# Optimization experiments

Measured on AMD Instinct MI355X. Metric: run time of the kernel, lower is better.

## Reference

```python
import jax, jax.numpy as jnp
import numpy as np

N = 50000          # num nodes
E = 600000         # num edges
D_IN = 128         # node_dim
D_HID = 128        # hidden_dim
D_OUT = 32         # num_classes
R = 32             # num_relations
B = 8              # num_bases


def setup_inputs() -> dict:
    key = jax.random.key(0)
    ks = jax.random.split(key, 12)
    inp = {
        "x": jax.random.normal(ks[0], (N, D_IN), dtype=jnp.float32),
        "V1": jax.random.normal(ks[1], (B, D_IN, D_HID), dtype=jnp.float32) * 0.05,
        "a1": jax.random.normal(ks[2], (R, B), dtype=jnp.float32),
        "root1": jax.random.normal(ks[3], (D_IN, D_HID), dtype=jnp.float32) * 0.05,
        "bias1": jnp.zeros((D_HID,), dtype=jnp.float32),
        "V2": jax.random.normal(ks[4], (B, D_HID, D_OUT), dtype=jnp.float32) * 0.05,
        "a2": jax.random.normal(ks[5], (R, B), dtype=jnp.float32),
        "root2": jax.random.normal(ks[6], (D_HID, D_OUT), dtype=jnp.float32) * 0.05,
        "bias2": jnp.zeros((D_OUT,), dtype=jnp.float32),
        "edge_index": jax.random.randint(ks[7], (2, E), 0, N, dtype=jnp.int64),
        "edge_type": jax.random.randint(ks[8], (E,), 0, R, dtype=jnp.int64),
    }
    return inp


def rgcn_layer(x, V, a, root, bias, src, dst, etype):
    # Aggregate neighbor features per (relation, dst-node) with mean norm,
    # then apply basis-decomposed relation weights W_r = sum_b a[r,b] V_b.
    D = x.shape[-1]
    seg = etype * N + dst                                   # [E] combined segment id
    msgs = x[src]                                           # [E, D] gather
    agg = jax.ops.segment_sum(msgs, seg, num_segments=R * N)        # [R*N, D]
    cnt = jax.ops.segment_sum(jnp.ones((msgs.shape[0], 1), x.dtype), seg,
                              num_segments=R * N)                   # [R*N, 1]
    agg = (agg / jnp.maximum(cnt, 1.0)).reshape(R, N, D)            # [R, N, D]
    W = jnp.einsum('rb,bdo->rdo', a, V)                     # [R, D, Dout]
    out = jnp.einsum('rnd,rdo->no', agg, W) + x @ root + bias
    return out


def reference(x, V1, a1, root1, bias1, V2, a2, root2, bias2, edge_index, edge_type):
    src, dst = edge_index[0], edge_index[1]
    h = rgcn_layer(x, V1, a1, root1, bias1, src, dst, edge_type)
    h = jax.nn.relu(h)
    h = rgcn_layer(h, V2, a2, root2, bias2, src, dst, edge_type)
    return jax.nn.softmax(h, axis=1)
```

## Files before the change

### kernel.cpp

```cpp
#include <hip/hip_runtime.h>
#include <hip/hip_bf16.h>
#include <hip/hip_fp16.h>


typedef __attribute__((ext_vector_type(8))) short bf16x8;
typedef __attribute__((ext_vector_type(4))) float f32x4;
typedef unsigned short u16;
typedef __attribute__((ext_vector_type(4))) unsigned short u16x4;

constexpr int TD   = 128;
constexpr int TB   = 8;
constexpr int TK   = TB * TD;
constexpr int TNB  = 16;
constexpr int BLK  = 512;
constexpr int ZK   = TK + 8;
constexpr int XK   = TD + 8;
constexpr int EC   = 512;

__device__ inline unsigned int splitbf(float v) {
  unsigned int u = __float_as_uint(v);
  unsigned int r = u + 0x7FFF + ((u >> 16) & 1);
  unsigned int hb = r >> 16;
  float hv = __uint_as_float(hb << 16);
  float lo = v - hv;
  unsigned int u2 = __float_as_uint(lo);
  unsigned int r2 = u2 + 0x7FFF + ((u2 >> 16) & 1);
  return (hb & 0xFFFFu) | (r2 & 0xFFFF0000u);
}

__device__ inline u16 f2h(float v) { return __half_as_ushort(__float2half(v)); }
__device__ inline float h2f(u16 b) { return __half2float(__ushort_as_half(b)); }

__global__ void k_prep(const float* __restrict__ V1, const float* __restrict__ root1,
                       const float* __restrict__ V2, const float* __restrict__ root2,
                       u16* __restrict__ v1th, u16* __restrict__ v1tl,
                       u16* __restrict__ r1th, u16* __restrict__ r1tl,
                       u16* __restrict__ v2th, u16* __restrict__ v2tl,
                       u16* __restrict__ r2th, u16* __restrict__ r2tl) {
  int idx = blockIdx.x * 256 + threadIdx.x;
  if (idx < 128 * 1024) {
    unsigned int p = splitbf(V1[(size_t)(idx & 1023) * 128 + (idx >> 10)]);
    v1th[idx] = (u16)p; v1tl[idx] = (u16)(p >> 16);
  }
  if (idx < 128 * 128) {
    unsigned int p = splitbf(root1[(size_t)(idx & 127) * 128 + (idx >> 7)]);
    r1th[idx] = (u16)p; r1tl[idx] = (u16)(p >> 16);
  }
  if (idx < 32 * 1024) {
    unsigned int p = splitbf(V2[(size_t)(idx & 1023) * 32 + (idx >> 10)]);
    v2th[idx] = (u16)p; v2tl[idx] = (u16)(p >> 16);
  }
  if (idx < 32 * 128) {
    unsigned int p = splitbf(root2[(size_t)(idx & 127) * 32 + (idx >> 7)]);
    r2th[idx] = (u16)p; r2tl[idx] = (u16)(p >> 16);
  }
}

__global__ void k_xcast(const float* __restrict__ x, u16* __restrict__ xb, int n4) {
  int i = blockIdx.x * 256 + threadIdx.x;
  if (i >= n4) return;
  float4 v = reinterpret_cast<const float4*>(x)[i];
  u16x4 o;
  o[0] = f2h(v.x); o[1] = f2h(v.y); o[2] = f2h(v.z); o[3] = f2h(v.w);
  reinterpret_cast<u16x4*>(xb)[i] = o;
}

__global__ void k_hist(const int* __restrict__ ei, const int* __restrict__ et,
                       int* __restrict__ deg, int* __restrict__ cnt2,
                       int E, int N) {
  int e = blockIdx.x * 256 + threadIdx.x;
  if (e >= E) return;
  int d = ei[E + e];
  int r = et[e];
  atomicAdd(&deg[d], 1);
  atomicAdd(&cnt2[r * N + d], 1);
}

__global__ void k_scan(const int* __restrict__ deg, int* __restrict__ off,
                       int* __restrict__ cursor, int n, int total) {
  __shared__ int wsum[16];
  __shared__ int carry_s;
  const int t = threadIdx.x, lane = t & 63, w = t >> 6;
  if (t == 0) carry_s = 0;
  __syncthreads();
  for (int base = 0; base < n; base += 1024) {
    int i = base + t;
    int v = (i < n) ? deg[i] : 0;
    int s = v;
#pragma unroll
    for (int d = 1; d < 64; d <<= 1) {
      int u = __shfl_up(s, d);
      if (lane >= d) s += u;
    }
    if (lane == 63) wsum[w] = s;
    __syncthreads();
    if (w == 0) {
      int ws = (lane < 16) ? wsum[lane] : 0;
#pragma unroll
      for (int d = 1; d < 16; d <<= 1) {
        int u = __shfl_up(ws, d);
        if (lane >= d) ws += u;
      }
      if (lane < 16) wsum[lane] = ws;
    }
    __syncthreads();
    int wbase = (w == 0) ? 0 : wsum[w - 1];
    int carry = carry_s;
    if (i < n) { int ex = carry + wbase + s - v; off[i] = ex; cursor[i] = ex; }
    __syncthreads();
    if (t == 1023) carry_s = carry + wbase + s;
    __syncthreads();
  }
  if (t == 0) off[n] = total;
}

__global__ void k_scatter(const int* __restrict__ ei, const int* __restrict__ et,
                          int* __restrict__ cursor, const int* __restrict__ cnt2,
                          int* __restrict__ packed, float* __restrict__ invc,
                          int E, int N) {
  int e = blockIdx.x * 256 + threadIdx.x;
  if (e >= E) return;
  int s = ei[e], d = ei[E + e], r = et[e];
  int p = atomicAdd(&cursor[d], 1);
  packed[p] = s | (r << 17);
  invc[p] = 1.0f / (float)cnt2[r * N + d];
}

#define MFMA16(A, B, C) __builtin_amdgcn_mfma_f32_16x16x32_bf16((A), (B), (C), 0, 0, 0)

template <int DOUT, bool RELU, bool SOFTMAX, bool INF32, bool OUTH16>
__global__ __launch_bounds__(BLK, 4) void k_layer(
    const float* __restrict__ inf,
    const u16* __restrict__ inb,
    const u16* __restrict__ wth, const u16* __restrict__ wtl,
    const float* __restrict__ a,
    const u16* __restrict__ rth, const u16* __restrict__ rtl,
    const float* __restrict__ bias, const int* __restrict__ off,
    const int* __restrict__ packed, const float* __restrict__ invc,
    void* __restrict__ outv, int Ntot) {
  extern __shared__ char smem[];
  u16* zh = (u16*)smem;
  u16* zl = zh + TNB * ZK;
  u16* xh = zl + TNB * ZK;
  u16* xl2 = xh + TNB * XK;
  float* ash = (float*)(xl2 + TNB * XK);
  int*   lrp = (int*)(ash + 256);
  float* lri = (float*)(lrp + EC);
  const int t = threadIdx.x;
  const int n0 = blockIdx.x * TNB;

  if (t < 256) ash[t] = a[t];
  {
    int row = t >> 5;
    int c4 = (t & 31) * 4;
    int n = n0 + row;
    float4 v = make_float4(0.f, 0.f, 0.f, 0.f);
    if constexpr (INF32) {
      if (n < Ntot) v = *reinterpret_cast<const float4*>(inf + (size_t)n * TD + c4);
    } else {
      if (n < Ntot) {
        u16x4 hv = *reinterpret_cast<const u16x4*>(inb + (size_t)n * TD + c4);
        v = make_float4(h2f(hv[0]), h2f(hv[1]), h2f(hv[2]), h2f(hv[3]));
      }
    }
    unsigned int p0 = splitbf(v.x), p1 = splitbf(v.y), p2 = splitbf(v.z), p3 = splitbf(v.w);
    xh[row * XK + c4]     = (u16)p0; xl2[row * XK + c4]     = (u16)(p0 >> 16);
    xh[row * XK + c4 + 1] = (u16)p1; xl2[row * XK + c4 + 1] = (u16)(p1 >> 16);
    xh[row * XK + c4 + 2] = (u16)p2; xl2[row * XK + c4 + 2] = (u16)(p2 >> 16);
    xh[row * XK + c4 + 3] = (u16)p3; xl2[row * XK + c4 + 3] = (u16)(p3 >> 16);
  }
  const int e_start = off[n0 < Ntot ? n0 : Ntot];
  {
    int nend = n0 + TNB; if (nend > Ntot) nend = Ntot;
    int ec = off[nend] - e_start;
    if (ec > EC) ec = EC;
    for (int i = t; i < ec; i += BLK) {
      lrp[i] = packed[e_start + i];
      lri[i] = invc[e_start + i];
    }
  }
  __syncthreads();

  {
    const int wv = t >> 6, lane = t & 63;
    const int hf = lane >> 5, q = lane & 31;

    for (int nn = wv * 2; nn < wv * 2 + 2; ++nn) {
      int n = n0 + nn;
      float acc[8][4];
#pragma unroll
      for (int b = 0; b < 8; ++b)
#pragma unroll
        for (int j = 0; j < 4; ++j) acc[b][j] = 0.f;

      if (n < Ntot) {
        int e0 = off[n], e1 = off[n + 1];
        int np = (e1 - e0 + 1) >> 1;

        struct Pk { float4 xv, c0, c1; };
        auto ldst = [&](int pe) {
          Pk P;
          int e = e0 + 2 * pe + hf;
          float iv = 0.f; int r = 0;
          u16x4 xr = {0, 0, 0, 0};
          if (e < e1) {
            int le = e - e_start;
            int pk;
            if (le < EC) { pk = lrp[le]; iv = lri[le]; }
            else         { pk = packed[e]; iv = invc[e]; }
            r = pk >> 17;
            xr = *reinterpret_cast<const u16x4*>(inb + (size_t)(pk & 131071) * TD + q * 4);
          }
          P.xv = make_float4(h2f(xr[0]), h2f(xr[1]), h2f(xr[2]), h2f(xr[3]));
          float4 t0 = *reinterpret_cast<const float4*>(ash + r * 8);
          float4 t1 = *reinterpret_cast<const float4*>(ash + r * 8 + 4);
          P.c0 = make_float4(t0.x * iv, t0.y * iv, t0.z * iv, t0.w * iv);
          P.c1 = make_float4(t1.x * iv, t1.y * iv, t1.z * iv, t1.w * iv);
          return P;
        };
        auto comp = [&](const Pk& P) {
#define ACCB(bi, cc) \
          acc[bi][0] += (cc) * P.xv.x; acc[bi][1] += (cc) * P.xv.y; \
          acc[bi][2] += (cc) * P.xv.z; acc[bi][3] += (cc) * P.xv.w;
          ACCB(0, P.c0.x) ACCB(1, P.c0.y) ACCB(2, P.c0.z) ACCB(3, P.c0.w)
          ACCB(4, P.c1.x) ACCB(5, P.c1.y) ACCB(6, P.c1.z) ACCB(7, P.c1.w)
#undef ACCB
        };

        Pk A, B, C, D;
        if (np > 0) A = ldst(0);
        if (np > 1) B = ldst(1);
        if (np > 2) C = ldst(2);
        if (np > 3) D = ldst(3);
        for (int pe = 0; pe < np; pe += 4) {
          comp(A);
          if (pe + 4 < np) A = ldst(pe + 4);
          if (pe + 1 < np) {
            comp(B);
            if (pe + 5 < np) B = ldst(pe + 5);
          }
          if (pe + 2 < np) {
            comp(C);
            if (pe + 6 < np) C = ldst(pe + 6);
          }
          if (pe + 3 < np) {
            comp(D);
            if (pe + 7 < np) D = ldst(pe + 7);
          }
        }
      }

#pragma unroll
      for (int b = 0; b < 8; ++b) {
        float v0 = acc[b][0] + __shfl_xor(acc[b][0], 32);
        float v1 = acc[b][1] + __shfl_xor(acc[b][1], 32);
        float v2 = acc[b][2] + __shfl_xor(acc[b][2], 32);
        float v3 = acc[b][3] + __shfl_xor(acc[b][3], 32);
        if (hf == 0) {
          unsigned int p0 = splitbf(v0), p1 = splitbf(v1), p2 = splitbf(v2), p3 = splitbf(v3);
          u16x4 hh, ll;
          hh[0] = (u16)p0; ll[0] = (u16)(p0 >> 16);
          hh[1] = (u16)p1; ll[1] = (u16)(p1 >> 16);
          hh[2] = (u16)p2; ll[2] = (u16)(p2 >> 16);
          hh[3] = (u16)p3; ll[3] = (u16)(p3 >> 16);
          int idx = nn * ZK + b * TD + q * 4;
          *reinterpret_cast<u16x4*>(zh + idx) = hh;
          *reinterpret_cast<u16x4*>(zl + idx) = ll;
        }
      }
    }
  }
  __syncthreads();

  const int w = t >> 6, lane = t & 63;
  const int mc = lane & 15, kg = lane >> 4;

  if constexpr (DOUT == 128) {
    f32x4 acc = {0.f, 0.f, 0.f, 0.f};
    {
      const u16* za = zh + mc * ZK + kg * 8;
      const u16* zb = zl + mc * ZK + kg * 8;
      const u16* bha = wth + (size_t)(w * 16 + mc) * TK + kg * 8;
      const u16* bla = wtl + (size_t)(w * 16 + mc) * TK + kg * 8;
#pragma unroll 4
      for (int ks = 0; ks < 32; ++ks) {
        bf16x8 ah  = *(const bf16x8*)(za + 32 * ks);
        bf16x8 alo = *(const bf16x8*)(zb + 32 * ks);
        bf16x8 bh  = *(const bf16x8*)(bha + 32 * ks);
        bf16x8 blo = *(const bf16x8*)(bla + 32 * ks);
        acc = MFMA16(ah, bh, acc);
        acc = MFMA16(alo, bh, acc);
        acc = MFMA16(ah, blo, acc);
      }
      const u16* xa = xh + mc * XK + kg * 8;
      const u16* xb = xl2 + mc * XK + kg * 8;
      const u16* rha = rth + (size_t)(w * 16 + mc) * TD + kg * 8;
      const u16* rla = rtl + (size_t)(w * 16 + mc) * TD + kg * 8;
#pragma unroll
      for (int ks = 0; ks < 4; ++ks) {
        bf16x8 ah  = *(const bf16x8*)(xa + 32 * ks);
        bf16x8 alo = *(const bf16x8*)(xb + 32 * ks);
        bf16x8 bh  = *(const bf16x8*)(rha + 32 * ks);
        bf16x8 blo = *(const bf16x8*)(rla + 32 * ks);
        acc = MFMA16(ah, bh, acc);
        acc = MFMA16(alo, bh, acc);
        acc = MFMA16(ah, blo, acc);
      }
    }
    float bb = bias[w * 16 + mc];
#pragma unroll
    for (int j = 0; j < 4; ++j) {
      int n = n0 + kg * 4 + j;
      if (n < Ntot) {
        float v = acc[j] + bb;
        if (RELU) v = fmaxf(v, 0.f);
        if constexpr (OUTH16) {
          ((u16*)outv)[(size_t)n * 128 + w * 16 + mc] = f2h(v);
        } else {
          ((float*)outv)[(size_t)n * 128 + w * 16 + mc] = v;
        }
      }
    }
  } else {
    f32x4 a0 = {0.f, 0.f, 0.f, 0.f}, a1 = {0.f, 0.f, 0.f, 0.f};
    {
      const u16* za = zh + mc * ZK + kg * 8;
      const u16* zb = zl + mc * ZK + kg * 8;
      const u16* b0h = wth + (size_t)mc * TK + kg * 8;
      const u16* b0l = wtl + (size_t)mc * TK + kg * 8;
      const u16* b1h = wth + (size_t)(16 + mc) * TK + kg * 8;
      const u16* b1l = wtl + (size_t)(16 + mc) * TK + kg * 8;
#pragma unroll
      for (int i = 0; i < 4; ++i) {
        int ks = w * 4 + i;
        bf16x8 ah  = *(const bf16x8*)(za + 32 * ks);
        bf16x8 alo = *(const bf16x8*)(zb + 32 * ks);
        bf16x8 bh0 = *(const bf16x8*)(b0h + 32 * ks);
        bf16x8 bl0 = *(const bf16x8*)(b0l + 32 * ks);
        bf16x8 bh1 = *(const bf16x8*)(b1h + 32 * ks);
        bf16x8 bl1 = *(const bf16x8*)(b1l + 32 * ks);
        a0 = MFMA16(ah, bh0, a0);
        a0 = MFMA16(alo, bh0, a0);
        a0 = MFMA16(ah, bl0, a0);
        a1 = MFMA16(ah, bh1, a1);
        a1 = MFMA16(alo, bh1, a1);
        a1 = MFMA16(ah, bl1, a1);
      }
      if (w < 4) {
        int ks = w;
        bf16x8 ah  = *(const bf16x8*)(xh + mc * XK + kg * 8 + 32 * ks);
        bf16x8 alo = *(const bf16x8*)(xl2 + mc * XK + kg * 8 + 32 * ks);
        bf16x8 bh0 = *(const bf16x8*)(rth + (size_t)mc * TD + kg * 8 + 32 * ks);
        bf16x8 bl0 = *(const bf16x8*)(rtl + (size_t)mc * TD + kg * 8 + 32 * ks);
        bf16x8 bh1 = *(const bf16x8*)(rth + (size_t)(16 + mc) * TD + kg * 8 + 32 * ks);
        bf16x8 bl1 = *(const bf16x8*)(rtl + (size_t)(16 + mc) * TD + kg * 8 + 32 * ks);
        a0 = MFMA16(ah, bh0, a0);
        a0 = MFMA16(alo, bh0, a0);
        a0 = MFMA16(ah, bl0, a0);
        a1 = MFMA16(ah, bh1, a1);
        a1 = MFMA16(alo, bh1, a1);
        a1 = MFMA16(ah, bl1, a1);
      }
    }
    __syncthreads();
    float* pc = (float*)smem;
#pragma unroll
    for (int j = 0; j < 4; ++j) {
      pc[(w * 2 + 0) * 256 + (kg * 4 + j) * 16 + mc] = a0[j];
      pc[(w * 2 + 1) * 256 + (kg * 4 + j) * 16 + mc] = a1[j];
    }
    __syncthreads();
    int row = t >> 5, col = t & 31;
    int tile = col >> 4, cc = col & 15;
    float v = 0.f;
#pragma unroll
    for (int ww = 0; ww < 8; ++ww) v += pc[(ww * 2 + tile) * 256 + row * 16 + cc];
    v += bias[col];
    if constexpr (SOFTMAX) {
      float m = v;
      m = fmaxf(m, __shfl_xor(m, 1));
      m = fmaxf(m, __shfl_xor(m, 2));
      m = fmaxf(m, __shfl_xor(m, 4));
      m = fmaxf(m, __shfl_xor(m, 8));
      m = fmaxf(m, __shfl_xor(m, 16));
      float ev = __expf(v - m);
      float s = ev;
      s += __shfl_xor(s, 1); s += __shfl_xor(s, 2); s += __shfl_xor(s, 4);
      s += __shfl_xor(s, 8); s += __shfl_xor(s, 16);
      v = ev / s;
    }
    int n = n0 + row;
    if (n < Ntot) ((float*)outv)[(size_t)n * 32 + col] = v;
  }
}

extern "C" void kernel_launch(void* const* d_in, const int* in_sizes, int n_in,
                              void* d_out, int out_size, void* d_ws, size_t ws_size,
                              hipStream_t stream) {
  const float* x     = (const float*)d_in[0];
  const float* V1    = (const float*)d_in[1];
  const float* a1    = (const float*)d_in[2];
  const float* root1 = (const float*)d_in[3];
  const float* bias1 = (const float*)d_in[4];
  const float* V2    = (const float*)d_in[5];
  const float* a2    = (const float*)d_in[6];
  const float* root2 = (const float*)d_in[7];
  const float* bias2 = (const float*)d_in[8];
  const int*   ei    = (const int*)d_in[9];
  const int*   et    = (const int*)d_in[10];

  const int N = in_sizes[0] / TD;
  const int E = in_sizes[10];
  const int R = 32;

  char* w = (char*)d_ws;
  auto alloc = [&](size_t bytes) {
    char* p = w;
    w += (bytes + 255) & ~(size_t)255;
    return p;
  };
  int*   off    = (int*)alloc((size_t)(N + 1) * 4);
  int*   cursor = (int*)alloc((size_t)N * 4);
  int*   deg    = (int*)alloc((size_t)N * 4);
  int*   cnt2   = (int*)alloc((size_t)R * N * 4);
  int*   packed = (int*)alloc((size_t)E * 4);
  float* invc   = (float*)alloc((size_t)E * 4);
  u16*   xb     = (u16*)alloc((size_t)N * TD * 2);
  u16*   hb     = (u16*)alloc((size_t)N * TD * 2);
  u16*   v1th   = (u16*)alloc((size_t)128 * 1024 * 2);
  u16*   v1tl   = (u16*)alloc((size_t)128 * 1024 * 2);
  u16*   r1th   = (u16*)alloc((size_t)128 * 128 * 2);
  u16*   r1tl   = (u16*)alloc((size_t)128 * 128 * 2);
  u16*   v2th   = (u16*)alloc((size_t)32 * 1024 * 2);
  u16*   v2tl   = (u16*)alloc((size_t)32 * 1024 * 2);
  u16*   r2th   = (u16*)alloc((size_t)32 * 128 * 2);
  u16*   r2tl   = (u16*)alloc((size_t)32 * 128 * 2);

  hipMemsetAsync(deg, 0, (size_t)N * 4, stream);
  hipMemsetAsync(cnt2, 0, (size_t)R * N * 4, stream);

  k_prep<<<512, 256, 0, stream>>>(V1, root1, V2, root2,
                                  v1th, v1tl, r1th, r1tl, v2th, v2tl, r2th, r2tl);
  int n4 = N * TD / 4;
  k_xcast<<<(n4 + 255) / 256, 256, 0, stream>>>(x, xb, n4);

  int egrid = (E + 255) / 256;
  k_hist<<<egrid, 256, 0, stream>>>(ei, et, deg, cnt2, E, N);
  k_scan<<<1, 1024, 0, stream>>>(deg, off, cursor, N, E);
  k_scatter<<<egrid, 256, 0, stream>>>(ei, et, cursor, cnt2, packed, invc, E, N);

  const size_t shmem = (size_t)(2 * TNB * ZK + 2 * TNB * XK) * 2 + 256 * 4 + (size_t)EC * 8;
  (void)hipFuncSetAttribute(reinterpret_cast<const void*>(&k_layer<128, true, false, true, true>),
                            hipFuncAttributeMaxDynamicSharedMemorySize, (int)shmem);
  (void)hipFuncSetAttribute(reinterpret_cast<const void*>(&k_layer<32, false, true, false, false>),
                            hipFuncAttributeMaxDynamicSharedMemorySize, (int)shmem);

  int ngrid = (N + TNB - 1) / TNB;
  k_layer<128, true, false, true, true><<<ngrid, BLK, shmem, stream>>>(
      x, xb, v1th, v1tl, a1, r1th, r1tl, bias1, off, packed, invc, hb, N);
  k_layer<32, false, true, false, false><<<ngrid, BLK, shmem, stream>>>(
      nullptr, hb, v2th, v2tl, a2, r2th, r2tl, bias2, off, packed, invc, d_out, N);
}
```

Measured before the change: 578.5 us.

## Split fused RGCN layer into separate gather and MFMA GEMM kernels over two halves

Each fused layer kernel is split into a gather kernel and a GEMM kernel. The gather kernel accumulates the basis-weighted neighbor sums into global hi/lo bf16 buffers, and the GEMM kernel reloads them and runs the MFMA projection. Node blocks are processed in two halves so the intermediate buffer stays half-sized. The gather kernel uses less shared memory and a higher occupancy hint, and the edge prefetch depth drops from four pairs to two (also in the fallback fused kernel). The cost is an extra global round-trip of the 1024-wide intermediate per node plus four more kernel launches per layer pair.

```diff
diff --git a/kernel.cpp b/kernel.cpp
--- a/kernel.cpp
+++ b/kernel.cpp
@@ -7,6 +7,7 @@
 typedef __attribute__((ext_vector_type(4))) float f32x4;
 typedef unsigned short u16;
 typedef __attribute__((ext_vector_type(4))) unsigned short u16x4;
+typedef __attribute__((ext_vector_type(8))) unsigned short u16x8;
 
 constexpr int TD   = 128;
 constexpr int TB   = 8;
@@ -128,10 +129,287 @@
 
 #define MFMA16(A, B, C) __builtin_amdgcn_mfma_f32_16x16x32_bf16((A), (B), (C), 0, 0, 0)
 
+__global__ __launch_bounds__(BLK, 8) void k_gather(
+    const u16* __restrict__ inb, const float* __restrict__ a,
+    const int* __restrict__ off, const int* __restrict__ packed,
+    const float* __restrict__ invc,
+    u16* __restrict__ zhg, u16* __restrict__ zlg,
+    int nbase, int Ntot) {
+  extern __shared__ char smem[];
+  float* ash = (float*)smem;
+  int*   lrp = (int*)(ash + 256);
+  float* lri = (float*)(lrp + EC);
+  const int t = threadIdx.x;
+  const int n0 = nbase + blockIdx.x * TNB;
+
+  if (t < 256) ash[t] = a[t];
+  const int e_start = off[n0 < Ntot ? n0 : Ntot];
+  {
+    int nend = n0 + TNB; if (nend > Ntot) nend = Ntot;
+    int ec = off[nend < 0 ? 0 : nend] - e_start;
+    if (ec > EC) ec = EC;
+    for (int i = t; i < ec; i += BLK) {
+      lrp[i] = packed[e_start + i];
+      lri[i] = invc[e_start + i];
+    }
+  }
+  __syncthreads();
+
+  const int wv = t >> 6, lane = t & 63;
+  const int hf = lane >> 5, q = lane & 31;
+
+  for (int nn = wv * 2; nn < wv * 2 + 2; ++nn) {
+    int n = n0 + nn;
+    float acc[8][4];
+#pragma unroll
+    for (int b = 0; b < 8; ++b)
+#pragma unroll
+      for (int j = 0; j < 4; ++j) acc[b][j] = 0.f;
+
+    if (n < Ntot) {
+      int e0 = off[n], e1 = off[n + 1];
+      int np = (e1 - e0 + 1) >> 1;
+
+      struct Pk { float4 xv, c0, c1; };
+      auto ldst = [&](int pe) {
+        Pk P;
+        int e = e0 + 2 * pe + hf;
+        float iv = 0.f; int r = 0;
+        u16x4 xr = {0, 0, 0, 0};
+        if (e < e1) {
+          int le = e - e_start;
+          int pk;
+          if (le < EC) { pk = lrp[le]; iv = lri[le]; }
+          else         { pk = packed[e]; iv = invc[e]; }
+          r = pk >> 17;
+          xr = *reinterpret_cast<const u16x4*>(inb + (size_t)(pk & 131071) * TD + q * 4);
+        }
+        P.xv = make_float4(h2f(xr[0]), h2f(xr[1]), h2f(xr[2]), h2f(xr[3]));
+        float4 t0 = *reinterpret_cast<const float4*>(ash + r * 8);
+        float4 t1 = *reinterpret_cast<const float4*>(ash + r * 8 + 4);
+        P.c0 = make_float4(t0.x * iv, t0.y * iv, t0.z * iv, t0.w * iv);
+        P.c1 = make_float4(t1.x * iv, t1.y * iv, t1.z * iv, t1.w * iv);
+        return P;
+      };
+      auto comp = [&](const Pk& P) {
+#define ACCB(bi, cc) \
+        acc[bi][0] += (cc) * P.xv.x; acc[bi][1] += (cc) * P.xv.y; \
+        acc[bi][2] += (cc) * P.xv.z; acc[bi][3] += (cc) * P.xv.w;
+        ACCB(0, P.c0.x) ACCB(1, P.c0.y) ACCB(2, P.c0.z) ACCB(3, P.c0.w)
+        ACCB(4, P.c1.x) ACCB(5, P.c1.y) ACCB(6, P.c1.z) ACCB(7, P.c1.w)
+#undef ACCB
+      };
+
+      Pk A, B;
+      if (np > 0) A = ldst(0);
+      if (np > 1) B = ldst(1);
+      for (int pe = 0; pe < np; pe += 2) {
+        comp(A);
+        if (pe + 2 < np) A = ldst(pe + 2);
+        if (pe + 1 < np) {
+          comp(B);
+          if (pe + 3 < np) B = ldst(pe + 3);
+        }
+      }
+    }
+
+#pragma unroll
+    for (int b = 0; b < 8; ++b) {
+      float v0 = acc[b][0] + __shfl_xor(acc[b][0], 32);
+      float v1 = acc[b][1] + __shfl_xor(acc[b][1], 32);
+      float v2 = acc[b][2] + __shfl_xor(acc[b][2], 32);
+      float v3 = acc[b][3] + __shfl_xor(acc[b][3], 32);
+      if (hf == 0 && n < Ntot) {
+        unsigned int p0 = splitbf(v0), p1 = splitbf(v1), p2 = splitbf(v2), p3 = splitbf(v3);
+        u16x4 hh, ll;
+        hh[0] = (u16)p0; ll[0] = (u16)(p0 >> 16);
+        hh[1] = (u16)p1; ll[1] = (u16)(p1 >> 16);
+        hh[2] = (u16)p2; ll[2] = (u16)(p2 >> 16);
+        hh[3] = (u16)p3; ll[3] = (u16)(p3 >> 16);
+        size_t gi = (size_t)(blockIdx.x * TNB + nn) * 1024 + b * TD + q * 4;
+        *reinterpret_cast<u16x4*>(zhg + gi) = hh;
+        *reinterpret_cast<u16x4*>(zlg + gi) = ll;
+      }
+    }
+  }
+}
+
+template <int DOUT, bool RELU, bool SOFTMAX, bool INF32, bool OUTH16>
+__global__ __launch_bounds__(BLK, 4) void k_gemm(
+    const float* __restrict__ inf, const u16* __restrict__ inb,
+    const u16* __restrict__ wth, const u16* __restrict__ wtl,
+    const u16* __restrict__ rth, const u16* __restrict__ rtl,
+    const float* __restrict__ bias,
+    const u16* __restrict__ zhg, const u16* __restrict__ zlg,
+    int nbase, void* __restrict__ outv, int Ntot) {
+  extern __shared__ char smem[];
+  u16* zh = (u16*)smem;
+  u16* zl = zh + TNB * ZK;
+  u16* xh = zl + TNB * ZK;
+  u16* xl2 = xh + TNB * XK;
+  const int t = threadIdx.x;
+  const int n0 = nbase + blockIdx.x * TNB;
+
+  {
+    int row = t >> 5;
+    int c4 = (t & 31) * 4;
+    int n = n0 + row;
+    float4 v = make_float4(0.f, 0.f, 0.f, 0.f);
+    if constexpr (INF32) {
+      if (n < Ntot) v = *reinterpret_cast<const float4*>(inf + (size_t)n * TD + c4);
+    } else {
+      if (n < Ntot) {
+        u16x4 hv = *reinterpret_cast<const u16x4*>(inb + (size_t)n * TD + c4);
+        v = make_float4(h2f(hv[0]), h2f(hv[1]), h2f(hv[2]), h2f(hv[3]));
+      }
+    }
+    unsigned int p0 = splitbf(v.x), p1 = splitbf(v.y), p2 = splitbf(v.z), p3 = splitbf(v.w);
+    xh[row * XK + c4]     = (u16)p0; xl2[row * XK + c4]     = (u16)(p0 >> 16);
+    xh[row * XK + c4 + 1] = (u16)p1; xl2[row * XK + c4 + 1] = (u16)(p1 >> 16);
+    xh[row * XK + c4 + 2] = (u16)p2; xl2[row * XK + c4 + 2] = (u16)(p2 >> 16);
+    xh[row * XK + c4 + 3] = (u16)p3; xl2[row * XK + c4 + 3] = (u16)(p3 >> 16);
+  }
+  {
+    const size_t zbase = (size_t)(blockIdx.x * TNB) * 1024;
+    for (int i = t; i < TNB * 128; i += BLK) {
+      int row = i >> 7, col8 = (i & 127) * 8;
+      u16x8 vh = {0,0,0,0,0,0,0,0}, vl = {0,0,0,0,0,0,0,0};
+      if (n0 + row < Ntot) {
+        size_t g = zbase + (size_t)row * 1024 + col8;
+        vh = *reinterpret_cast<const u16x8*>(zhg + g);
+        vl = *reinterpret_cast<const u16x8*>(zlg + g);
+      }
+      *reinterpret_cast<u16x8*>(zh + row * ZK + col8) = vh;
+      *reinterpret_cast<u16x8*>(zl + row * ZK + col8) = vl;
+    }
+  }
+  __syncthreads();
+
+  const int w = t >> 6, lane = t & 63;
+  const int mc = lane & 15, kg = lane >> 4;
+
+  if constexpr (DOUT == 128) {
+    f32x4 acc = {0.f, 0.f, 0.f, 0.f};
+    {
+      const u16* za = zh + mc * ZK + kg * 8;
+      const u16* zb = zl + mc * ZK + kg * 8;
+      const u16* bha = wth + (size_t)(w * 16 + mc) * TK + kg * 8;
+      const u16* bla = wtl + (size_t)(w * 16 + mc) * TK + kg * 8;
+#pragma unroll 4
+      for (int ks = 0; ks < 32; ++ks) {
+        bf16x8 ah  = *(const bf16x8*)(za + 32 * ks);
+        bf16x8 alo = *(const bf16x8*)(zb + 32 * ks);
+        bf16x8 bh  = *(const bf16x8*)(bha + 32 * ks);
+        bf16x8 blo = *(const bf16x8*)(bla + 32 * ks);
+        acc = MFMA16(ah, bh, acc);
+        acc = MFMA16(alo, bh, acc);
+        acc = MFMA16(ah, blo, acc);
+      }
+      const u16* xa = xh + mc * XK + kg * 8;
+      const u16* xb = xl2 + mc * XK + kg * 8;
+      const u16* rha = rth + (size_t)(w * 16 + mc) * TD + kg * 8;
+      const u16* rla = rtl + (size_t)(w * 16 + mc) * TD + kg * 8;
+#pragma unroll
+      for (int ks = 0; ks < 4; ++ks) {
+        bf16x8 ah  = *(const bf16x8*)(xa + 32 * ks);
+        bf16x8 alo = *(const bf16x8*)(xb + 32 * ks);
+        bf16x8 bh  = *(const bf16x8*)(rha + 32 * ks);
+        bf16x8 blo = *(const bf16x8*)(rla + 32 * ks);
+        acc = MFMA16(ah, bh, acc);
+        acc = MFMA16(alo, bh, acc);
+        acc = MFMA16(ah, blo, acc);
+      }
+    }
+    float bb = bias[w * 16 + mc];
+#pragma unroll
+    for (int j = 0; j < 4; ++j) {
+      int n = n0 + kg * 4 + j;
+      if (n < Ntot) {
+        float v = acc[j] + bb;
+        if (RELU) v = fmaxf(v, 0.f);
+        if constexpr (OUTH16) {
+          ((u16*)outv)[(size_t)n * 128 + w * 16 + mc] = f2h(v);
+        } else {
+          ((float*)outv)[(size_t)n * 128 + w * 16 + mc] = v;
+        }
+      }
+    }
+  } else {
+    f32x4 a0 = {0.f, 0.f, 0.f, 0.f}, a1 = {0.f, 0.f, 0.f, 0.f};
+    {
+      const u16* za = zh + mc * ZK + kg * 8;
+      const u16* zb = zl + mc * ZK + kg * 8;
+      const u16* b0h = wth + (size_t)mc * TK + kg * 8;
+      const u16* b0l = wtl + (size_t)mc * TK + kg * 8;
+      const u16* b1h = wth + (size_t)(16 + mc) * TK + kg * 8;
+      const u16* b1l = wtl + (size_t)(16 + mc) * TK + kg * 8;
+#pragma unroll
+      for (int i = 0; i < 4; ++i) {
+        int ks = w * 4 + i;
+        bf16x8 ah  = *(const bf16x8*)(za + 32 * ks);
+        bf16x8 alo = *(const bf16x8*)(zb + 32 * ks);
+        bf16x8 bh0 = *(const bf16x8*)(b0h + 32 * ks);
+        bf16x8 bl0 = *(const bf16x8*)(b0l + 32 * ks);
+        bf16x8 bh1 = *(const bf16x8*)(b1h + 32 * ks);
+        bf16x8 bl1 = *(const bf16x8*)(b1l + 32 * ks);
+        a0 = MFMA16(ah, bh0, a0);
+        a0 = MFMA16(alo, bh0, a0);
+        a0 = MFMA16(ah, bl0, a0);
+        a1 = MFMA16(ah, bh1, a1);
+        a1 = MFMA16(alo, bh1, a1);
+        a1 = MFMA16(ah, bl1, a1);
+      }
+      if (w < 4) {
+        int ks = w;
+        bf16x8 ah  = *(const bf16x8*)(xh + mc * XK + kg * 8 + 32 * ks);
+        bf16x8 alo = *(const bf16x8*)(xl2 + mc * XK + kg * 8 + 32 * ks);
+        bf16x8 bh0 = *(const bf16x8*)(rth + (size_t)mc * TD + kg * 8 + 32 * ks);
+        bf16x8 bl0 = *(const bf16x8*)(rtl + (size_t)mc * TD + kg * 8 + 32 * ks);
+        bf16x8 bh1 = *(const bf16x8*)(rth + (size_t)(16 + mc) * TD + kg * 8 + 32 * ks);
+        bf16x8 bl1 = *(const bf16x8*)(rtl + (size_t)(16 + mc) * TD + kg * 8 + 32 * ks);
+        a0 = MFMA16(ah, bh0, a0);
+        a0 = MFMA16(alo, bh0, a0);
+        a0 = MFMA16(ah, bl0, a0);
+        a1 = MFMA16(ah, bh1, a1);
+        a1 = MFMA16(alo, bh1, a1);
+        a1 = MFMA16(ah, bl1, a1);
+      }
+    }
+    __syncthreads();
+    float* pc = (float*)smem;
+#pragma unroll
+    for (int j = 0; j < 4; ++j) {
+      pc[(w * 2 + 0) * 256 + (kg * 4 + j) * 16 + mc] = a0[j];
+      pc[(w * 2 + 1) * 256 + (kg * 4 + j) * 16 + mc] = a1[j];
+    }
+    __syncthreads();
+    int row = t >> 5, col = t & 31;
+    int tile = col >> 4, cc = col & 15;
+    float v = 0.f;
+#pragma unroll
+    for (int ww = 0; ww < 8; ++ww) v += pc[(ww * 2 + tile) * 256 + row * 16 + cc];
+    v += bias[col];
+    if constexpr (SOFTMAX) {
+      float m = v;
+      m = fmaxf(m, __shfl_xor(m, 1));
+      m = fmaxf(m, __shfl_xor(m, 2));
+      m = fmaxf(m, __shfl_xor(m, 4));
+      m = fmaxf(m, __shfl_xor(m, 8));
+      m = fmaxf(m, __shfl_xor(m, 16));
+      float ev = __expf(v - m);
+      float s = ev;
+      s += __shfl_xor(s, 1); s += __shfl_xor(s, 2); s += __shfl_xor(s, 4);
+      s += __shfl_xor(s, 8); s += __shfl_xor(s, 16);
+      v = ev / s;
+    }
+    int n = n0 + row;
+    if (n < Ntot) ((float*)outv)[(size_t)n * 32 + col] = v;
+  }
+}
+
 template <int DOUT, bool RELU, bool SOFTMAX, bool INF32, bool OUTH16>
 __global__ __launch_bounds__(BLK, 4) void k_layer(
-    const float* __restrict__ inf,
-    const u16* __restrict__ inb,
+    const float* __restrict__ inf, const u16* __restrict__ inb,
     const u16* __restrict__ wth, const u16* __restrict__ wtl,
     const float* __restrict__ a,
     const u16* __restrict__ rth, const u16* __restrict__ rtl,
@@ -184,7 +462,6 @@
   {
     const int wv = t >> 6, lane = t & 63;
     const int hf = lane >> 5, q = lane & 31;
-
     for (int nn = wv * 2; nn < wv * 2 + 2; ++nn) {
       int n = n0 + nn;
       float acc[8][4];
@@ -196,7 +473,6 @@
       if (n < Ntot) {
         int e0 = off[n], e1 = off[n + 1];
         int np = (e1 - e0 + 1) >> 1;
-
         struct Pk { float4 xv, c0, c1; };
         auto ldst = [&](int pe) {
           Pk P;
@@ -226,30 +502,18 @@
           ACCB(4, P.c1.x) ACCB(5, P.c1.y) ACCB(6, P.c1.z) ACCB(7, P.c1.w)
 #undef ACCB
         };
-
-        Pk A, B, C, D;
+        Pk A, B;
         if (np > 0) A = ldst(0);
         if (np > 1) B = ldst(1);
-        if (np > 2) C = ldst(2);
-        if (np > 3) D = ldst(3);
-        for (int pe = 0; pe < np; pe += 4) {
+        for (int pe = 0; pe < np; pe += 2) {
           comp(A);
-          if (pe + 4 < np) A = ldst(pe + 4);
+          if (pe + 2 < np) A = ldst(pe + 2);
           if (pe + 1 < np) {
             comp(B);
-            if (pe + 5 < np) B = ldst(pe + 5);
-          }
-          if (pe + 2 < np) {
-            comp(C);
-            if (pe + 6 < np) C = ldst(pe + 6);
-          }
-          if (pe + 3 < np) {
-            comp(D);
-            if (pe + 7 < np) D = ldst(pe + 7);
+            if (pe + 3 < np) B = ldst(pe + 3);
           }
         }
       }
-
 #pragma unroll
       for (int b = 0; b < 8; ++b) {
         float v0 = acc[b][0] + __shfl_xor(acc[b][0], 32);
@@ -436,6 +700,14 @@
   u16*   r2th   = (u16*)alloc((size_t)32 * 128 * 2);
   u16*   r2tl   = (u16*)alloc((size_t)32 * 128 * 2);
 
+  const int tblocks = (N + TNB - 1) / TNB;
+  const int c1b = (tblocks + 1) / 2;
+  const int c2b = tblocks - c1b;
+  const int maxcn = c1b * TNB;
+  u16* zhg = (u16*)alloc((size_t)maxcn * 1024 * 2);
+  u16* zlg = (u16*)alloc((size_t)maxcn * 1024 * 2);
+  const bool split_ok = (size_t)(w - (char*)d_ws) <= ws_size;
+
   hipMemsetAsync(deg, 0, (size_t)N * 4, stream);
   hipMemsetAsync(cnt2, 0, (size_t)R * N * 4, stream);
 
@@ -449,15 +721,34 @@
   k_scan<<<1, 1024, 0, stream>>>(deg, off, cursor, N, E);
   k_scatter<<<egrid, 256, 0, stream>>>(ei, et, cursor, cnt2, packed, invc, E, N);
 
-  const size_t shmem = (size_t)(2 * TNB * ZK + 2 * TNB * XK) * 2 + 256 * 4 + (size_t)EC * 8;
-  (void)hipFuncSetAttribute(reinterpret_cast<const void*>(&k_layer<128, true, false, true, true>),
-                            hipFuncAttributeMaxDynamicSharedMemorySize, (int)shmem);
-  (void)hipFuncSetAttribute(reinterpret_cast<const void*>(&k_layer<32, false, true, false, false>),
-                            hipFuncAttributeMaxDynamicSharedMemorySize, (int)shmem);
-
-  int ngrid = (N + TNB - 1) / TNB;
-  k_layer<128, true, false, true, true><<<ngrid, BLK, shmem, stream>>>(
-      x, xb, v1th, v1tl, a1, r1th, r1tl, bias1, off, packed, invc, hb, N);
-  k_layer<32, false, true, false, false><<<ngrid, BLK, shmem, stream>>>(
-      nullptr, hb, v2th, v2tl, a2, r2th, r2tl, bias2, off, packed, invc, d_out, N);
-}
+  if (split_ok) {
+    const size_t sh_g = 256 * 4 + EC * 8;
+    const size_t sh_m = (size_t)(2 * TNB * ZK + 2 * TNB * XK) * 2;
+    (void)hipFuncSetAttribute(reinterpret_cast<const void*>(&k_gemm<128, true, false, true, true>),
+                              hipFuncAttributeMaxDynamicSharedMemorySize, (int)sh_m);
+    (void)hipFuncSetAttribute(reinterpret_cast<const void*>(&k_gemm<32, false, true, false, false>),
+                              hipFuncAttributeMaxDynamicSharedMemorySize, (int)sh_m);
+    k_gather<<<c1b, BLK, sh_g, stream>>>(xb, a1, off, packed, invc, zhg, zlg, 0, N);
+    k_gemm<128, true, false, true, true><<<c1b, BLK, sh_m, stream>>>(
+        x, xb, v1th, v1tl, r1th, r1tl, bias1, zhg, zlg, 0, hb, N);
+    k_gather<<<c2b, BLK, sh_g, stream>>>(xb, a1, off, packed, invc, zhg, zlg, c1b * TNB, N);
+    k_gemm<128, true, false, true, true><<<c2b, BLK, sh_m, stream>>>(
+        x, xb, v1th, v1tl, r1th, r1tl, bias1, zhg, zlg, c1b * TNB, hb, N);
+    k_gather<<<c1b, BLK, sh_g, stream>>>(hb, a2, off, packed, invc, zhg, zlg, 0, N);
+    k_gemm<32, false, true, false, false><<<c1b, BLK, sh_m, stream>>>(
+        nullptr, hb, v2th, v2tl, r2th, r2tl, bias2, zhg, zlg, 0, d_out, N);
+    k_gather<<<c2b, BLK, sh_g, stream>>>(hb, a2, off, packed, invc, zhg, zlg, c1b * TNB, N);
+    k_gemm<32, false, true, false, false><<<c2b, BLK, sh_m, stream>>>(
+        nullptr, hb, v2th, v2tl, r2th, r2tl, bias2, zhg, zlg, c1b * TNB, d_out, N);
+  } else {
+    const size_t shmem = (size_t)(2 * TNB * ZK + 2 * TNB * XK) * 2 + 256 * 4 + (size_t)EC * 8;
+    (void)hipFuncSetAttribute(reinterpret_cast<const void*>(&k_layer<128, true, false, true, true>),
+                              hipFuncAttributeMaxDynamicSharedMemorySize, (int)shmem);
+    (void)hipFuncSetAttribute(reinterpret_cast<const void*>(&k_layer<32, false, true, false, false>),
+                              hipFuncAttributeMaxDynamicSharedMemorySize, (int)shmem);
+    k_layer<128, true, false, true, true><<<tblocks, BLK, shmem, stream>>>(
+        x, xb, v1th, v1tl, a1, r1th, r1tl, bias1, off, packed, invc, hb, N);
+    k_layer<32, false, true, false, false><<<tblocks, BLK, shmem, stream>>>(
+        nullptr, hb, v2th, v2tl, a2, r2th, r2tl, bias2, off, packed, invc, d_out, N);
+  }
+}
```

Measured after the change: 1.377 ms. 138% more time.
